# Optimization experiments

Measured on AMD Instinct MI355X. Metric: run time of the kernel, lower is better.

## Reference

```python
import jax, jax.numpy as jnp
import numpy as np

B_SZ = 4; SEQ = 2048; D_INPUT = 40; D_MODEL = 128; N_LAYERS = 4
D_STATE = 16; EXPAND = 2; D_INNER = D_MODEL * EXPAND
N_HEADS = 4; D_HEAD = D_MODEL // N_HEADS; MAX_LANDMARKS = 100
EPS_RMS = 1.1920929e-07  # torch nn.RMSNorm default eps = finfo(float32).eps
EPS_LN = 1e-5
A_FLOOR = 1e-4


def _rms(x, w):
    return x * jax.lax.rsqrt(jnp.mean(x * x, -1, keepdims=True) + EPS_RMS) * w


def _ln(x, w, b):
    m = jnp.mean(x, -1, keepdims=True)
    v = jnp.mean((x - m) ** 2, -1, keepdims=True)
    return (x - m) * jax.lax.rsqrt(v + EPS_LN) * w + b


def _mamba3_block(xin, Wi, Wx, Wdt, bdt, Alog, Bb, Cb, Bnw, Cnw, rf, Dv, Wo):
    # xin: (B,L,d_model)
    xz = xin @ Wi                       # (B,L,2*d_inner)
    xp, z = jnp.split(xz, 2, axis=-1)
    xp = jax.nn.silu(xp)
    sp = xp @ Wx                        # (B,L,2*d_state+2)
    B_raw = sp[..., :D_STATE]
    C_raw = sp[..., D_STATE:2 * D_STATE]
    dt_in = sp[..., -2:-1]
    lam_in = sp[..., -1:]
    Bm = _rms(B_raw + Bb, Bnw)
    Cm = _rms(C_raw + Cb, Cnw)
    dt = jax.nn.softplus(dt_in @ Wdt + bdt)   # (B,L,d_inner)
    lam = jax.nn.sigmoid(lam_in)              # (B,L,1)
    # data-dependent RoPE on B and C
    freqs = jax.nn.softplus(rf)                                  # (d_state//2,)
    ang = jnp.cumsum(jnp.mean(dt, -1, keepdims=True), axis=1) * freqs  # (B,L,ds/2)
    ca, sa = jnp.cos(ang), jnp.sin(ang)

    def rot(M):
        e, o = M[..., ::2], M[..., 1::2]
        return jnp.stack([e * ca - o * sa, e * sa + o * ca], -1).reshape(M.shape)

    Bm, Cm = rot(Bm), rot(Cm)
    A = jnp.minimum(-jnp.exp(Alog), -A_FLOOR)   # (d_inner,d_state)
    dte = dt[..., None]                          # (B,L,d_inner,1)
    dA = jnp.exp(A * dte)                        # (B,L,d_inner,d_state)
    Bx = Bm[:, :, None, :] * xp[..., None]       # (B,L,d_inner,d_state)
    Bx_prev = jnp.concatenate([jnp.zeros_like(Bx[:, :1]), Bx[:, :-1]], axis=1)
    lame = lam[..., None]                        # (B,L,1,1)
    u = (1.0 - lame) * dte * dA * Bx_prev + lame * dte * Bx
    u = u.at[:, 0].set(dte[:, 0] * Bx[:, 0])     # t==0 case: h = dt*B*x (no lambda)

    def step(h, inp):
        dA_t, u_t, C_t = inp
        h = dA_t * h + u_t
        return h, jnp.sum(h * C_t[:, None, :], -1)

    h0 = jnp.zeros((xin.shape[0], D_INNER, D_STATE), xin.dtype)
    _, ys = jax.lax.scan(step, h0, (jnp.swapaxes(dA, 0, 1), jnp.swapaxes(u, 0, 1), jnp.swapaxes(Cm, 0, 1)))
    y = jnp.swapaxes(ys, 0, 1)                   # (B,L,d_inner)
    y = y + xp * Dv
    y = y * jax.nn.silu(z)
    return y @ Wo


def _landmark_attn(mo, skip, hw, WQ, bQ, WK, bK, WV, bV, WO, bO):
    Bsz, L, Dm = skip.shape
    k = min(MAX_LANDMARKS, L)
    _, idx = jax.lax.top_k(hw, k)
    idx = jnp.sort(idx, axis=1)                            # (B,k)
    kv = jnp.take_along_axis(skip, idx[..., None], axis=1)  # (B,k,Dm)
    q = mo[:, -1:, :]                                       # (B,1,Dm)
    Q = (q @ WQ + bQ).reshape(Bsz, 1, N_HEADS, D_HEAD).transpose(0, 2, 1, 3)
    K = (kv @ WK + bK).reshape(Bsz, k, N_HEADS, D_HEAD).transpose(0, 2, 1, 3)
    V = (kv @ WV + bV).reshape(Bsz, k, N_HEADS, D_HEAD).transpose(0, 2, 1, 3)
    scores = jnp.einsum('bhqd,bhkd->bhqk', Q, K) * (D_HEAD ** -0.5)
    probs = jax.nn.softmax(scores, axis=-1)
    out = jnp.einsum('bhqk,bhkd->bhqd', probs, V).transpose(0, 2, 1, 3).reshape(Bsz, Dm)
    return out @ WO + bO


def setup_inputs() -> dict:
    key = jax.random.key(0)
    ks = iter(jax.random.split(key, 64))

    def nrm(shape, s=0.02):
        return jax.random.normal(next(ks), shape, jnp.float32) * s

    nl, ds, di, dm = N_LAYERS, D_STATE, D_INNER, D_MODEL
    inp = {}
    inp['x'] = jax.random.normal(next(ks), (B_SZ, SEQ, D_INPUT), jnp.float32)
    inp['hawkes_weights'] = jax.random.uniform(next(ks), (B_SZ, SEQ), jnp.float32)
    inp['emb_W'] = nrm((D_INPUT, dm)); inp['emb_b'] = jnp.zeros(dm, jnp.float32)
    inp['skip_W'] = nrm((D_INPUT, dm)); inp['skip_b'] = jnp.zeros(dm, jnp.float32)
    inp['in_proj_W'] = nrm((nl, dm, 2 * di))
    inp['x_proj_W'] = nrm((nl, di, 2 * ds + 2))
    inp['dt_proj_W'] = nrm((nl, 1, di), 1.0)
    inp['dt_proj_b'] = jnp.full((nl, di), -1.0, jnp.float32)
    inp['A_log'] = jnp.broadcast_to(jnp.log(jnp.arange(1, ds + 1, dtype=jnp.float32)), (nl, di, ds)) * jnp.ones((nl, di, ds), jnp.float32)
    inp['B_bias'] = jnp.ones((nl, ds), jnp.float32)
    inp['C_bias'] = jnp.ones((nl, ds), jnp.float32)
    inp['Bn_w'] = jnp.ones((nl, ds), jnp.float32)
    inp['Cn_w'] = jnp.ones((nl, ds), jnp.float32)
    inp['rope_freqs'] = nrm((nl, ds // 2), 0.01)
    inp['D_param'] = jnp.ones((nl, di), jnp.float32)
    inp['out_proj_W'] = nrm((nl, di, dm))
    inp['ln_w'] = jnp.ones((nl, dm), jnp.float32); inp['ln_b'] = jnp.zeros((nl, dm), jnp.float32)
    inp['fn_w'] = jnp.ones(dm, jnp.float32); inp['fn_b'] = jnp.zeros(dm, jnp.float32)
    for nm in ('Q', 'K', 'V', 'O'):
        inp['W' + nm] = nrm((dm, dm)); inp['b' + nm] = jnp.zeros(dm, jnp.float32)
    return inp


def reference(x, hawkes_weights, emb_W, emb_b, skip_W, skip_b, in_proj_W, x_proj_W,
              dt_proj_W, dt_proj_b, A_log, B_bias, C_bias, Bn_w, Cn_w, rope_freqs,
              D_param, out_proj_W, ln_w, ln_b, fn_w, fn_b, WQ, bQ, WK, bK, WV, bV, WO, bO):
    w = hawkes_weights[..., None]
    h = (x @ emb_W + emb_b) * w          # Hawkes-damped embedding for Mamba path
    skip = (x @ skip_W + skip_b) * w     # Hawkes skip for attention KV
    for i in range(N_LAYERS):
        h = h + _mamba3_block(_ln(h, ln_w[i], ln_b[i]), in_proj_W[i], x_proj_W[i],
                              dt_proj_W[i], dt_proj_b[i], A_log[i], B_bias[i], C_bias[i],
                              Bn_w[i], Cn_w[i], rope_freqs[i], D_param[i], out_proj_W[i])
    mo = _ln(h, fn_w, fn_b)
    return _landmark_attn(mo, skip, hawkes_weights, WQ, bQ, WK, bK, WV, bV, WO, bO)
```

## Files before the change

kernel.cpp:

```cpp
#include <hip/hip_runtime.h>
#include <hip/hip_fp16.h>
#include <math.h>

#define BSZ   4
#define SEQL  2048
#define DIN   40
#define DM    128
#define DI    256
#define DS    16
#define NL    4
#define NHEAD 4
#define DHEAD 32
#define KLM   100
#define NC    128
#define TC    16
#define NROWS 8
#define EROWS 16

__device__ __forceinline__ float rcp_(float x){ return __builtin_amdgcn_rcpf(x); }
__device__ __forceinline__ float sigmoidf_(float x){ return rcp_(1.0f + __expf(-x)); }
__device__ __forceinline__ float siluf_(float x){ return x*rcp_(1.0f + __expf(-x)); }
__device__ __forceinline__ float softplusf_(float x){ return fmaxf(x,0.0f) + __logf(1.0f + __expf(-fabsf(x))); }

__device__ __forceinline__ float block_sum256(float v, float* red){
  #pragma unroll
  for (int o=32;o>0;o>>=1) v += __shfl_down(v,o,64);
  __syncthreads();
  if ((threadIdx.x & 63)==0) red[threadIdx.x>>6] = v;
  __syncthreads();
  return red[0]+red[1]+red[2]+red[3];
}
__device__ __forceinline__ void load8(const float* p, float* r){
  const float4* q = (const float4*)p;
  float4 a=q[0], b=q[1];
  r[0]=a.x;r[1]=a.y;r[2]=a.z;r[3]=a.w; r[4]=b.x;r[5]=b.y;r[6]=b.z;r[7]=b.w;
}
__device__ __forceinline__ void store8(float* p, const float* r){
  float4* q = (float4*)p;
  q[0]=make_float4(r[0],r[1],r[2],r[3]);  q[1]=make_float4(r[4],r[5],r[6],r[7]);
}
__device__ __forceinline__ void load16(const float* p, float* r){
  load8(p, r); load8(p+8, r+8);
}
__device__ __forceinline__ void store16(float* p, const float* r){
  store8(p, r); store8(p+8, r+8);
}

__global__ __launch_bounds__(256) void embed_kernel(
    const float* __restrict__ x, const float* __restrict__ hw,
    const float* __restrict__ eW, const float* __restrict__ eb,
    const float* __restrict__ sW, const float* __restrict__ sb,
    float* __restrict__ hb, float* __restrict__ sk)
{
  __shared__ float xr[EROWS][DIN];
  const int t = threadIdx.x;
  const size_t R0 = (size_t)blockIdx.x * EROWS;
  for (int e=t; e<EROWS*DIN; e+=256) ((float*)xr)[e] = x[R0*DIN + e];
  __syncthreads();
  const int c = t & (DM-1), g = t >> 7;
  float ae[8], as[8];
  #pragma unroll
  for (int j=0;j<8;j++){ ae[j]=0.0f; as[j]=0.0f; }
  for (int k=0;k<DIN;k++){
    const float we  = eW[(size_t)k*DM + c];
    const float ws_ = sW[(size_t)k*DM + c];
    #pragma unroll
    for (int j=0;j<8;j++){
      const float xv = xr[g*8+j][k];
      ae[j] = fmaf(xv, we, ae[j]);
      as[j] = fmaf(xv, ws_, as[j]);
    }
  }
  const float ebv = eb[c], sbv = sb[c];
  #pragma unroll
  for (int j=0;j<8;j++){
    const size_t R = R0 + g*8 + j;
    const float w = hw[R];
    hb[R*DM + c] = (ae[j]+ebv)*w;
    sk[R*DM + c] = (as[j]+sbv)*w;
  }
}

__global__ __launch_bounds__(256) void pre_kernel(
    const float* __restrict__ hb,
    const float* __restrict__ Wi, const float* __restrict__ Wx,
    const float* __restrict__ Wdt, const float* __restrict__ bdt,
    const float* __restrict__ Bb, const float* __restrict__ Cb,
    const float* __restrict__ Bnw, const float* __restrict__ Cnw,
    const float* __restrict__ lnw, const float* __restrict__ lnb,
    __half* __restrict__ xph, __half* __restrict__ zsh,
    float* __restrict__ dtin, float* __restrict__ Shalf,
    float* __restrict__ Bmb, float* __restrict__ Cmb,
    float* __restrict__ lamb, float* __restrict__ mdtb)
{
  __shared__ float xin[NROWS][DM+4];
  __shared__ float xps[NROWS][DI+4];
  __shared__ float spl[NROWS][40];
  __shared__ float pr[NROWS][4];

  const int t = threadIdx.x;
  const size_t R0 = (size_t)blockIdx.x * NROWS;

  {
    const int r = t >> 5, j = t & 31;
    const float4 v = ((const float4*)(hb + (R0 + r)*DM))[j];
    float s = v.x+v.y+v.z+v.w;
    #pragma unroll
    for (int o=16;o>0;o>>=1) s += __shfl_xor(s,o,32);
    const float m = s*(1.0f/DM);
    const float dx=v.x-m, dy=v.y-m, dz=v.z-m, dw=v.w-m;
    float ss = dx*dx+dy*dy+dz*dz+dw*dw;
    #pragma unroll
    for (int o=16;o>0;o>>=1) ss += __shfl_xor(ss,o,32);
    const float inv = 1.0f/sqrtf(ss*(1.0f/DM) + 1e-5f);
    const int c = j*4;
    xin[r][c+0] = dx*inv*lnw[c+0] + lnb[c+0];
    xin[r][c+1] = dy*inv*lnw[c+1] + lnb[c+1];
    xin[r][c+2] = dz*inv*lnw[c+2] + lnb[c+2];
    xin[r][c+3] = dw*inv*lnw[c+3] + lnb[c+3];
  }
  __syncthreads();

  {
    float2 a[NROWS];
    #pragma unroll
    for (int r=0;r<NROWS;r++){ a[r].x=0.0f; a[r].y=0.0f; }
    for (int k=0;k<DM;k+=4){
      const float2 w0 = *(const float2*)&Wi[(size_t)(k+0)*(2*DI) + 2*t];
      const float2 w1 = *(const float2*)&Wi[(size_t)(k+1)*(2*DI) + 2*t];
      const float2 w2 = *(const float2*)&Wi[(size_t)(k+2)*(2*DI) + 2*t];
      const float2 w3 = *(const float2*)&Wi[(size_t)(k+3)*(2*DI) + 2*t];
      #pragma unroll
      for (int r=0;r<NROWS;r++){
        const float4 xv = *(const float4*)&xin[r][k];
        a[r].x = fmaf(xv.x,w0.x,a[r].x); a[r].y = fmaf(xv.x,w0.y,a[r].y);
        a[r].x = fmaf(xv.y,w1.x,a[r].x); a[r].y = fmaf(xv.y,w1.y,a[r].y);
        a[r].x = fmaf(xv.z,w2.x,a[r].x); a[r].y = fmaf(xv.z,w2.y,a[r].y);
        a[r].x = fmaf(xv.w,w3.x,a[r].x); a[r].y = fmaf(xv.w,w3.y,a[r].y);
      }
    }
    if (t < 128){
      #pragma unroll
      for (int r=0;r<NROWS;r++){
        const float sx = siluf_(a[r].x), sy = siluf_(a[r].y);
        xps[r][2*t] = sx; xps[r][2*t+1] = sy;
        *(__half2*)&xph[(R0+r)*DI + 2*t] =
            __halves2half2(__float2half_rn(sx), __float2half_rn(sy));
      }
    } else {
      const int zc = 2*t - 2*DI + DI;
      #pragma unroll
      for (int r=0;r<NROWS;r++){
        const float sx = siluf_(a[r].x), sy = siluf_(a[r].y);
        *(__half2*)&zsh[(R0+r)*DI + zc] =
            __halves2half2(__float2half_rn(sx), __float2half_rn(sy));
      }
    }
  }
  __syncthreads();

  if (t < 136){
    const int r = t & 7, op = t >> 3;
    float ax=0.0f, ay=0.0f;
    for (int k=0;k<DI;k+=4){
      const float4 xv = *(const float4*)&xps[r][k];
      const float2 w0 = *(const float2*)&Wx[(size_t)(k+0)*34 + 2*op];
      const float2 w1 = *(const float2*)&Wx[(size_t)(k+1)*34 + 2*op];
      const float2 w2 = *(const float2*)&Wx[(size_t)(k+2)*34 + 2*op];
      const float2 w3 = *(const float2*)&Wx[(size_t)(k+3)*34 + 2*op];
      ax = fmaf(xv.x,w0.x,ax); ay = fmaf(xv.x,w0.y,ay);
      ax = fmaf(xv.y,w1.x,ax); ay = fmaf(xv.y,w1.y,ay);
      ax = fmaf(xv.z,w2.x,ax); ay = fmaf(xv.z,w2.y,ay);
      ax = fmaf(xv.w,w3.x,ax); ay = fmaf(xv.w,w3.y,ay);
    }
    spl[r][2*op] = ax; spl[r][2*op+1] = ay;
  }
  __syncthreads();

  {
    const int half = t >> 7;
    const int r2 = (t >> 4) & 7, s2 = t & 15;
    const float* bias = half ? Cb : Bb;
    const float* wn   = half ? Cnw : Bnw;
    const float v = spl[r2][half*DS + s2] + bias[s2];
    float ss = v*v;
    #pragma unroll
    for (int o=8;o>0;o>>=1) ss += __shfl_xor(ss,o,16);
    const float inv = 1.0f/sqrtf(ss*(1.0f/DS) + 1.1920929e-07f);
    (half ? Cmb : Bmb)[(R0+r2)*DS + s2] = v*inv*wn[s2];
  }

  {
    const int lane = t & 63, w = t >> 6;
    const float wdt = Wdt[t], bdtv = bdt[t];
    float Sd = 0.0f;
    #pragma unroll
    for (int r=0;r<NROWS;r++){
      const float dval = softplusf_(fmaf(spl[r][32], wdt, bdtv));
      Sd += dval;
      float s = dval;
      #pragma unroll
      for (int o=32;o>0;o>>=1) s += __shfl_xor(s,o,64);
      if (lane==0) pr[r][w] = s;
    }
    Shalf[(size_t)blockIdx.x * DI + t] = Sd;
    if (t < NROWS){
      lamb[R0+t] = sigmoidf_(spl[t][33]);
      dtin[R0+t] = spl[t][32];
    }
  }
  __syncthreads();
  if (t < NROWS)
    mdtb[R0+t] = (pr[t][0]+pr[t][1]+pr[t][2]+pr[t][3])*(1.0f/DI);
}

__global__ __launch_bounds__(256) void cumsum_kernel(
    const float* __restrict__ mdt, double* __restrict__ csum_g)
{
  __shared__ double wsum[4];
  const int b = blockIdx.x, t = threadIdx.x;
  const int lane = t & 63, w = t >> 6;
  const float* p = mdt + (size_t)b*SEQL + (size_t)t*8;
  double v[8]; double s = 0.0;
  #pragma unroll
  for (int q=0;q<8;q++){ v[q] = (double)p[q]; s += v[q]; }
  double sc = s;
  #pragma unroll
  for (int o=1;o<64;o<<=1){
    const double nb = __shfl_up(sc, o, 64);
    if (lane >= o) sc += nb;
  }
  if (lane==63) wsum[w] = sc;
  __syncthreads();
  double woff = 0.0;
  for (int j=0;j<w;j++) woff += wsum[j];
  double run = woff + sc - s;
  double* dst = csum_g + (size_t)b*SEQL + (size_t)t*8;
  #pragma unroll
  for (int q=0;q<8;q++){ run += v[q]; dst[q] = run; }
}

__global__ __launch_bounds__(256) void csfill_kernel(
    const double* __restrict__ csum_g, const float* __restrict__ rf,
    float2* __restrict__ cst)
{
  __shared__ double fqs[8];
  const int t = threadIdx.x;
  if (t < 8){
    const double xfr = (double)rf[t];
    fqs[t] = fmax(xfr, 0.0) + log1p(exp(-fabs(xfr)));
  }
  __syncthreads();
  const int row = blockIdx.x*256 + t;
  const double ab = csum_g[row];
  const double TWO_PI = 6.283185307179586;
  const double INV2PI = 0.15915494309189535;
  float2 o8[8];
  #pragma unroll
  for (int f=0; f<8; f++){
    const double ang = ab * fqs[f];
    const double red = ang - floor(ang*INV2PI)*TWO_PI;
    float sa, ca;
    __sincosf((float)red, &sa, &ca);
    o8[f] = make_float2(ca, sa);
  }
  float4* dst = (float4*)&cst[(size_t)row*8];
  dst[0] = make_float4(o8[0].x,o8[0].y,o8[1].x,o8[1].y);
  dst[1] = make_float4(o8[2].x,o8[2].y,o8[3].x,o8[3].y);
  dst[2] = make_float4(o8[4].x,o8[4].y,o8[5].x,o8[5].y);
  dst[3] = make_float4(o8[6].x,o8[6].y,o8[7].x,o8[7].y);
}

__global__ __launch_bounds__(512) void scan1_kernel(
    const __half* __restrict__ xph, const float* __restrict__ dtin,
    const float* __restrict__ Wdt, const float* __restrict__ bdt,
    const float* __restrict__ Bmb, const float* __restrict__ lamb,
    const float2* __restrict__ cst,
    const float* __restrict__ Alog, float* __restrict__ hend)
{
  __shared__ float Bst[TC+1][DS];
  __shared__ float lst[TC];
  __shared__ float dsl[TC];
  __shared__ __half xpl[TC+1][DI+8];
  const int t = threadIdx.x;
  const int d  = t >> 1;
  const int s0 = (t & 1) * 8;
  const int c = blockIdx.x & (NC-1);
  const int b = blockIdx.x >> 7;
  const size_t bL = (size_t)b*SEQL;
  const int t0 = c*TC;
  const int id = blockIdx.x*256 + d;

  for (int e=t; e<(TC+1)*DS; e+=512){
    const int j = e >> 4, s = e & 15;
    const int trow = t0 - 1 + j;
    Bst[j][s] = (trow >= 0) ? Bmb[(bL + trow)*DS + s] : 0.0f;
  }
  for (int e=t; e<(TC+1)*DI; e+=512){
    const int j = e >> 8, dd = e & (DI-1);
    const int trow = t0 - 1 + j;
    xpl[j][dd] = (trow >= 0) ? xph[(bL + trow)*DI + dd] : __float2half_rn(0.0f);
  }
  if (t < TC){
    lst[t] = lamb[bL + t0 + t];
    dsl[t] = dtin[bL + t0 + t];
  }
  __syncthreads();
  if (t < 136){
    const int j = t >> 3, f = t & 7;
    const int trow = t0 - 1 + j;
    if (trow >= 0){
      const float2 cs = cst[((size_t)(bL + trow))*8 + f];
      const float e0 = Bst[j][2*f], o0 = Bst[j][2*f+1];
      Bst[j][2*f]   = e0*cs.x - o0*cs.y;
      Bst[j][2*f+1] = e0*cs.y + o0*cs.x;
    }
  }
  __syncthreads();

  float A[8];
  #pragma unroll
  for (int s=0;s<8;s++) A[s] = fminf(-__expf(Alog[d*DS + s0 + s]), -1e-4f);
  const float wdt = Wdt[d], bdtv = bdt[d];
  float h[8], Bprev[8];
  #pragma unroll
  for (int s=0;s<8;s++) h[s]=0.0f;
  float xpm1;
  int tstart;
  if (t0 > 0){
    #pragma unroll
    for (int s=0;s<8;s++) Bprev[s] = Bst[0][s0+s];
    xpm1 = __half2float(xpl[0][d]);
    tstart = t0;
  } else {
    const float dtv = softplusf_(fmaf(dsl[0], wdt, bdtv));
    const float xpv = __half2float(xpl[1][d]);
    #pragma unroll
    for (int s=0;s<8;s++){
      h[s] = dtv*(Bst[1][s0+s]*xpv);
      Bprev[s] = Bst[1][s0+s];
    }
    xpm1 = xpv;
    tstart = 1;
  }
  for (int tt=tstart; tt<t0+TC; ++tt){
    const int j = tt - t0;
    const float dtv = softplusf_(fmaf(dsl[j], wdt, bdtv));
    const float xpv = __half2float(xpl[j+1][d]);
    const float lamv = lst[j];
    const float dl = dtv*lamv;
    const float dml = dtv - dl;
    #pragma unroll
    for (int s=0;s<8;s++){
      const float a = __expf(A[s]*dtv);
      const float Bc = Bst[j+1][s0+s];
      const float u = fmaf(dml*a, Bprev[s]*xpm1, dl*(Bc*xpv));
      h[s] = fmaf(a, h[s], u);
      Bprev[s] = Bc;
    }
    xpm1 = xpv;
  }
  store8(hend + (size_t)id*DS + s0, h);
}

__global__ __launch_bounds__(128) void scan2_kernel(
    float* __restrict__ hend, const float* __restrict__ Shalf,
    const float* __restrict__ Alog)
{
  __shared__ float hS[NC][DS+1];
  __shared__ float pS[NC][DS+1];
  const int c = threadIdx.x;
  const int d = blockIdx.x & (DI-1);
  const int b = blockIdx.x >> 8;
  const float S = Shalf[(size_t)(b*(SEQL/NROWS) + 2*c)*DI + d]
                + Shalf[(size_t)(b*(SEQL/NROWS) + 2*c + 1)*DI + d];
  float P[DS], h[DS];
  #pragma unroll
  for (int s=0;s<DS;s++){
    const float A = fminf(-__expf(Alog[d*DS+s]), -1e-4f);
    P[s] = __expf(A*S);
  }
  load16(hend + (((size_t)(b*NC + c))*DI + d)*DS, h);
  #pragma unroll
  for (int s=0;s<DS;s++){ hS[c][s]=h[s]; pS[c][s]=P[s]; }
  __syncthreads();
  for (int off=1; off<NC; off<<=1){
    float hn[DS], pn[DS];
    const int src = c - off;
    if (src >= 0){
      #pragma unroll
      for (int s=0;s<DS;s++){ hn[s]=hS[src][s]; pn[s]=pS[src][s]; }
    }
    __syncthreads();
    if (src >= 0){
      #pragma unroll
      for (int s=0;s<DS;s++){
        h[s] = fmaf(P[s], hn[s], h[s]);
        P[s] *= pn[s];
        hS[c][s] = h[s]; pS[c][s] = P[s];
      }
    }
    __syncthreads();
  }
  float o[DS];
  if (c == 0){
    #pragma unroll
    for (int s=0;s<DS;s++) o[s] = 0.0f;
  } else {
    #pragma unroll
    for (int s=0;s<DS;s++) o[s] = hS[c-1][s];
  }
  store16(hend + (((size_t)(b*NC + c))*DI + d)*DS, o);
}

__global__ __launch_bounds__(512) void scan3post_kernel(
    const __half* __restrict__ xph, const float* __restrict__ dtin,
    const float* __restrict__ Wdt, const float* __restrict__ bdt,
    const float* __restrict__ Bmb, const float* __restrict__ Cmb,
    const float* __restrict__ lamb, const __half* __restrict__ zsh,
    const float2* __restrict__ cst,
    const float* __restrict__ Alog, const float* __restrict__ Dv,
    const float* __restrict__ Hin, const float* __restrict__ Wo,
    float* __restrict__ hb)
{
  __shared__ float Bst[TC+1][DS];
  __shared__ float Cst[TC][DS];
  __shared__ float lst[TC];
  __shared__ float dsl[TC];
  __shared__ __half xpl[TC+1][DI+8];
  __shared__ __half zsl[TC][DI+8];
  __shared__ float ys[TC][DI+4];
  const int t = threadIdx.x;
  const int d  = t >> 1;
  const int sh = t & 1;
  const int s0 = sh * 8;
  const int c = blockIdx.x & (NC-1);
  const int b = blockIdx.x >> 7;
  const size_t bL = (size_t)b*SEQL;
  const int t0 = c*TC;
  const int id = blockIdx.x*256 + d;

  for (int e=t; e<(TC+1)*DS; e+=512){
    const int j = e >> 4, s = e & 15;
    const int trow = t0 - 1 + j;
    Bst[j][s] = (trow >= 0) ? Bmb[(bL + trow)*DS + s] : 0.0f;
    if (j < TC) Cst[j][s] = Cmb[(bL + t0 + j)*DS + s];
  }
  for (int e=t; e<(TC+1)*DI; e+=512){
    const int j = e >> 8, dd = e & (DI-1);
    const int trow = t0 - 1 + j;
    xpl[j][dd] = (trow >= 0) ? xph[(bL + trow)*DI + dd] : __float2half_rn(0.0f);
    if (j < TC) zsl[j][dd] = zsh[(bL + t0 + j)*DI + dd];
  }
  if (t < TC){
    lst[t] = lamb[bL + t0 + t];
    dsl[t] = dtin[bL + t0 + t];
  }
  __syncthreads();
  if (t < 264){
    if (t < 136){
      const int j = t >> 3, f = t & 7;
      const int trow = t0 - 1 + j;
      if (trow >= 0){
        const float2 cs = cst[((size_t)(bL + trow))*8 + f];
        const float e0 = Bst[j][2*f], o0 = Bst[j][2*f+1];
        Bst[j][2*f]   = e0*cs.x - o0*cs.y;
        Bst[j][2*f+1] = e0*cs.y + o0*cs.x;
      }
    } else {
      const int e2 = t - 136;
      const int j = e2 >> 3, f = e2 & 7;
      const float2 cs = cst[((size_t)(bL + t0 + j))*8 + f];
      const float e0 = Cst[j][2*f], o0 = Cst[j][2*f+1];
      Cst[j][2*f]   = e0*cs.x - o0*cs.y;
      Cst[j][2*f+1] = e0*cs.y + o0*cs.x;
    }
  }
  __syncthreads();

  float A[8];
  #pragma unroll
  for (int s=0;s<8;s++) A[s] = fminf(-__expf(Alog[d*DS + s0 + s]), -1e-4f);
  const float wdt = Wdt[d], bdtv = bdt[d];
  const float dvp = Dv[d];
  float h[8], Bprev[8];
  load8(Hin + (size_t)id*DS + s0, h);
  float xpm1;
  int tstart;
  if (t0 > 0){
    #pragma unroll
    for (int s=0;s<8;s++) Bprev[s] = Bst[0][s0+s];
    xpm1 = __half2float(xpl[0][d]);
    tstart = t0;
  } else {
    const float dtv = softplusf_(fmaf(dsl[0], wdt, bdtv));
    const float xpv = __half2float(xpl[1][d]);
    float y = 0.0f;
    #pragma unroll
    for (int s=0;s<8;s++){
      h[s] = dtv*(Bst[1][s0+s]*xpv);
      y = fmaf(h[s], Cst[0][s0+s], y);
      Bprev[s] = Bst[1][s0+s];
    }
    const float ytot = y + __shfl_xor(y, 1, 64);
    if (sh == 0) ys[0][d] = (ytot + xpv*dvp)*__half2float(zsl[0][d]);
    xpm1 = xpv;
    tstart = 1;
  }
  for (int tt=tstart; tt<t0+TC; ++tt){
    const int j = tt - t0;
    const float dtv = softplusf_(fmaf(dsl[j], wdt, bdtv));
    const float xpv = __half2float(xpl[j+1][d]);
    const float lamv = lst[j];
    const float dl = dtv*lamv;
    const float dml = dtv - dl;
    float y = 0.0f;
    #pragma unroll
    for (int s=0;s<8;s++){
      const float a = __expf(A[s]*dtv);
      const float Bc = Bst[j+1][s0+s];
      const float u = fmaf(dml*a, Bprev[s]*xpm1, dl*(Bc*xpv));
      h[s] = fmaf(a, h[s], u);
      y = fmaf(h[s], Cst[j][s0+s], y);
      Bprev[s] = Bc;
    }
    const float ytot = y + __shfl_xor(y, 1, 64);
    if (sh == 0) ys[j][d] = (ytot + xpv*dvp)*__half2float(zsl[j][d]);
    xpm1 = xpv;
  }
  __syncthreads();

  {
    const int r  = t >> 5;
    const int cg = t & 31;
    const int c0 = cg*4;
    float acc[4] = {0.0f,0.0f,0.0f,0.0f};
    for (int k=0;k<DI;k+=4){
      const float4 yv = *(const float4*)&ys[r][k];
      const float yy[4] = {yv.x, yv.y, yv.z, yv.w};
      #pragma unroll
      for (int j=0;j<4;j++){
        const float4 wa = *(const float4*)&Wo[(size_t)(k+j)*DM + c0];
        acc[0]=fmaf(yy[j],wa.x,acc[0]); acc[1]=fmaf(yy[j],wa.y,acc[1]);
        acc[2]=fmaf(yy[j],wa.z,acc[2]); acc[3]=fmaf(yy[j],wa.w,acc[3]);
      }
    }
    const size_t row = bL + t0 + r;
    float4 h0 = *(const float4*)&hb[row*DM + c0];
    h0.x+=acc[0]; h0.y+=acc[1]; h0.z+=acc[2]; h0.w+=acc[3];
    *(float4*)&hb[row*DM + c0] = h0;
  }
}

__global__ __launch_bounds__(256) void topk_kernel(
    const float* __restrict__ hb, const float* __restrict__ hw,
    const float* __restrict__ fnw, const float* __restrict__ fnb,
    int* __restrict__ idxl_g, float* __restrict__ mog)
{
  __shared__ int redcnt[2][4];
  __shared__ int eqc[8][4], gtc[8][4];
  __shared__ float red_f[4];

  const int b = blockIdx.x;
  const int t = threadIdx.x;
  const int lane = t & 63, w = t >> 6;

  const float* hwp = hw + (size_t)b*SEQL;
  unsigned vb[8];
  #pragma unroll
  for (int q=0;q<8;q++) vb[q] = __float_as_uint(hwp[q*256 + t]);

  unsigned kth = 0u;
  for (int bit=31; bit>=0; --bit){
    const unsigned cand = kth | (1u << bit);
    int c0 = 0;
    #pragma unroll
    for (int q=0;q<8;q++) c0 += __popcll(__ballot(vb[q] >= cand));
    const int par = bit & 1;
    if (lane == 0) redcnt[par][w] = c0;
    __syncthreads();
    const int tot = redcnt[par][0]+redcnt[par][1]+redcnt[par][2]+redcnt[par][3];
    if (tot >= KLM) kth = cand;
  }

  unsigned long long beq[8], bgt[8];
  #pragma unroll
  for (int q=0;q<8;q++){
    beq[q] = __ballot(vb[q] == kth);
    bgt[q] = __ballot(vb[q] >  kth);
  }
  if (lane == 0){
    #pragma unroll
    for (int q=0;q<8;q++){ eqc[q][w] = __popcll(beq[q]); gtc[q][w] = __popcll(bgt[q]); }
  }
  __syncthreads();
  {
    int gtTot = 0;
    #pragma unroll
    for (int q=0;q<8;q++) gtTot += gtc[q][0]+gtc[q][1]+gtc[q][2]+gtc[q][3];
    const int need_eq = KLM - gtTot;
    const unsigned long long lmask = (lane==0) ? 0ull : ((~0ull) >> (64-lane));
    int eqPfx = 0, gtPfx = 0;
    #pragma unroll
    for (int q=0;q<8;q++){
      int eqWP = 0, gtWP = 0;
      for (int w2=0; w2<w; ++w2){ eqWP += eqc[q][w2]; gtWP += gtc[q][w2]; }
      const int eqBefore = eqPfx + eqWP + __popcll(beq[q] & lmask);
      const int gtBefore = gtPfx + gtWP + __popcll(bgt[q] & lmask);
      if (vb[q] > kth){
        const int pos = gtBefore + min(eqBefore, need_eq);
        if (pos < KLM) idxl_g[b*KLM + pos] = q*256 + t;
      } else if (vb[q] == kth && eqBefore < need_eq){
        const int pos = gtBefore + eqBefore;
        if (pos < KLM) idxl_g[b*KLM + pos] = q*256 + t;
      }
      eqPfx += eqc[q][0]+eqc[q][1]+eqc[q][2]+eqc[q][3];
      gtPfx += gtc[q][0]+gtc[q][1]+gtc[q][2]+gtc[q][3];
    }
  }

  {
    const float* hr = hb + ((size_t)b*SEQL + (SEQL-1))*DM;
    const float hv = (t < DM) ? hr[t] : 0.0f;
    const float ssum = block_sum256(hv, red_f);
    const float mean = ssum*(1.0f/DM);
    const float dv = (t < DM) ? (hv - mean) : 0.0f;
    const float vsum = block_sum256(dv*dv, red_f);
    const float inv = 1.0f/sqrtf(vsum*(1.0f/DM) + 1e-5f);
    if (t < DM) mog[b*DM + t] = dv*inv*fnw[t] + fnb[t];
  }
}

__global__ __launch_bounds__(256) void attnmid_kernel(
    const float* __restrict__ sk, const int* __restrict__ idxl_g,
    const float* __restrict__ mog,
    const float* __restrict__ WQ, const float* __restrict__ bQ,
    const float* __restrict__ WK, const float* __restrict__ bK,
    const float* __restrict__ WV, const float* __restrict__ bV,
    float* __restrict__ attnog)
{
  __shared__ float kv[KLM][DM+4];
  __shared__ float Qs[DHEAD];
  __shared__ float qk[DM];
  __shared__ float sc[KLM];
  __shared__ float pbar[DM];
  __shared__ float bterm_s;
  const int t = threadIdx.x;
  const int b = blockIdx.x >> 2, hh = blockIdx.x & 3;
  const int c0 = hh*DHEAD;

  for (int e=t; e<KLM*DM; e+=256){
    const int j = e >> 7, cc = e & (DM-1);
    kv[j][cc] = sk[((size_t)b*SEQL + idxl_g[b*KLM + j])*DM + cc];
  }
  if (t < DHEAD){
    float a = bQ[c0+t];
    #pragma unroll 4
    for (int k=0;k<DM;k++) a = fmaf(mog[b*DM+k], WQ[(size_t)k*DM + c0+t], a);
    Qs[t] = a;
  }
  __syncthreads();
  if (t < DM){
    float a = 0.0f;
    #pragma unroll
    for (int cc=0; cc<DHEAD; cc++) a = fmaf(WK[(size_t)t*DM + c0 + cc], Qs[cc], a);
    qk[t] = a;
  } else if (t == DM){
    float a = 0.0f;
    for (int cc=0; cc<DHEAD; cc++) a += bK[c0+cc]*Qs[cc];
    bterm_s = a;
  }
  __syncthreads();
  if (t < KLM){
    float a = bterm_s;
    for (int m=0;m<DM;m+=4){
      const float4 kvv = *(const float4*)&kv[t][m];
      const float4 qv  = *(const float4*)&qk[m];
      a = fmaf(kvv.x,qv.x,a); a = fmaf(kvv.y,qv.y,a);
      a = fmaf(kvv.z,qv.z,a); a = fmaf(kvv.w,qv.w,a);
    }
    sc[t] = a*0.17677669529663687f;
  }
  __syncthreads();
  if (t < 64){
    const int lane = t;
    const float v0 = (lane < KLM) ? sc[lane] : -3.0e38f;
    const float v1 = (lane+64 < KLM) ? sc[lane+64] : -3.0e38f;
    float mx = fmaxf(v0, v1);
    #pragma unroll
    for (int o2=32;o2>0;o2>>=1) mx = fmaxf(mx, __shfl_xor(mx,o2,64));
    const float e0 = (lane < KLM) ? __expf(v0-mx) : 0.0f;
    const float e1 = (lane+64 < KLM) ? __expf(v1-mx) : 0.0f;
    float sm = e0+e1;
    #pragma unroll
    for (int o2=32;o2>0;o2>>=1) sm += __shfl_xor(sm,o2,64);
    const float inv2 = rcp_(sm);
    if (lane < KLM) sc[lane] = e0*inv2;
    if (lane+64 < KLM) sc[lane+64] = e1*inv2;
  }
  __syncthreads();
  if (t < DM){
    float a = 0.0f;
    #pragma unroll 4
    for (int j=0;j<KLM;j++) a = fmaf(sc[j], kv[j][t], a);
    pbar[t] = a;
  }
  __syncthreads();
  if (t < DHEAD){
    const int cc = c0 + t;
    float a = bV[cc];
    #pragma unroll 4
    for (int m=0;m<DM;m++) a = fmaf(pbar[m], WV[(size_t)m*DM + cc], a);
    attnog[b*DM + cc] = a;
  }
}

__global__ __launch_bounds__(128) void attnout_kernel(
    const float* __restrict__ attnog, const float* __restrict__ WO,
    const float* __restrict__ bO, float* __restrict__ outp)
{
  __shared__ float ao[DM];
  const int b = blockIdx.x, t = threadIdx.x;
  ao[t] = attnog[b*DM + t];
  __syncthreads();
  float a = bO[t];
  #pragma unroll 4
  for (int c2=0;c2<DM;c2++) a = fmaf(ao[c2], WO[(size_t)c2*DM + t], a);
  outp[(size_t)b*DM + t] = a;
}

extern "C" void kernel_launch(void* const* d_in, const int* in_sizes, int n_in,
                              void* d_out, int out_size, void* d_ws, size_t ws_size,
                              hipStream_t stream)
{
  (void)in_sizes; (void)n_in; (void)out_size; (void)ws_size;
  const float* x    = (const float*)d_in[0];
  const float* hw   = (const float*)d_in[1];
  const float* embW = (const float*)d_in[2];
  const float* embB = (const float*)d_in[3];
  const float* skW  = (const float*)d_in[4];
  const float* skB  = (const float*)d_in[5];
  const float* inW  = (const float*)d_in[6];
  const float* xpW  = (const float*)d_in[7];
  const float* dtW  = (const float*)d_in[8];
  const float* dtB  = (const float*)d_in[9];
  const float* Alog = (const float*)d_in[10];
  const float* Bb   = (const float*)d_in[11];
  const float* Cb   = (const float*)d_in[12];
  const float* Bnw  = (const float*)d_in[13];
  const float* Cnw  = (const float*)d_in[14];
  const float* rf   = (const float*)d_in[15];
  const float* Dpar = (const float*)d_in[16];
  const float* outW = (const float*)d_in[17];
  const float* lnW  = (const float*)d_in[18];
  const float* lnB  = (const float*)d_in[19];
  const float* fnW  = (const float*)d_in[20];
  const float* fnB  = (const float*)d_in[21];
  const float* WQ = (const float*)d_in[22]; const float* bQ = (const float*)d_in[23];
  const float* WK = (const float*)d_in[24]; const float* bK = (const float*)d_in[25];
  const float* WV = (const float*)d_in[26]; const float* bV = (const float*)d_in[27];
  const float* WO = (const float*)d_in[28]; const float* bO = (const float*)d_in[29];

  float* ws = (float*)d_ws;
  size_t off = 0;
  float* hb    = ws + off; off += (size_t)BSZ*SEQL*DM;
  float* sk    = ws + off; off += (size_t)BSZ*SEQL*DM;
  __half* xph  = (__half*)(ws + off); off += (size_t)BSZ*SEQL*DI/2;
  __half* zsh  = (__half*)(ws + off); off += (size_t)BSZ*SEQL*DI/2;
  float* Bmb   = ws + off; off += (size_t)BSZ*SEQL*DS;
  float* Cmb   = ws + off; off += (size_t)BSZ*SEQL*DS;
  float* lamb  = ws + off; off += (size_t)BSZ*SEQL;
  float* mdtb  = ws + off; off += (size_t)BSZ*SEQL;
  float* dtin  = ws + off; off += (size_t)BSZ*SEQL;
  float* Shalf = ws + off; off += (size_t)BSZ*(SEQL/NROWS)*DI;
  float* hend  = ws + off; off += (size_t)BSZ*NC*DI*DS;
  float2* cst  = (float2*)(ws + off); off += (size_t)BSZ*SEQL*16;
  double* csum_g = (double*)(ws + off); off += (size_t)BSZ*SEQL*2;
  int* idxl_g  = (int*)(ws + off); off += (size_t)BSZ*KLM;
  float* mog   = ws + off; off += (size_t)BSZ*DM;
  float* attnog= ws + off; off += (size_t)BSZ*DM;

  embed_kernel<<<BSZ*SEQL/EROWS, 256, 0, stream>>>(x, hw, embW, embB, skW, skB, hb, sk);

  for (int i=0;i<NL;i++){
    pre_kernel<<<BSZ*SEQL/NROWS, 256, 0, stream>>>(hb,
        inW + (size_t)i*DM*2*DI, xpW + (size_t)i*DI*34,
        dtW + (size_t)i*DI, dtB + (size_t)i*DI,
        Bb + i*DS, Cb + i*DS, Bnw + i*DS, Cnw + i*DS,
        lnW + i*DM, lnB + i*DM,
        xph, zsh, dtin, Shalf, Bmb, Cmb, lamb, mdtb);
    cumsum_kernel<<<BSZ, 256, 0, stream>>>(mdtb, csum_g);
    csfill_kernel<<<BSZ*SEQL/256, 256, 0, stream>>>(csum_g, rf + i*8, cst);
    scan1_kernel<<<BSZ*NC, 512, 0, stream>>>(xph, dtin,
        dtW + (size_t)i*DI, dtB + (size_t)i*DI,
        Bmb, lamb, cst, Alog + (size_t)i*DI*DS, hend);
    scan2_kernel<<<BSZ*DI, 128, 0, stream>>>(hend, Shalf, Alog + (size_t)i*DI*DS);
    scan3post_kernel<<<BSZ*NC, 512, 0, stream>>>(xph, dtin,
        dtW + (size_t)i*DI, dtB + (size_t)i*DI,
        Bmb, Cmb, lamb, zsh, cst,
        Alog + (size_t)i*DI*DS, Dpar + (size_t)i*DI, hend,
        outW + (size_t)i*DI*DM, hb);
  }

  topk_kernel<<<BSZ, 256, 0, stream>>>(hb, hw, fnW, fnB, idxl_g, mog);
  attnmid_kernel<<<BSZ*NHEAD, 256, 0, stream>>>(sk, idxl_g, mog,
      WQ, bQ, WK, bK, WV, bV, attnog);
  attnout_kernel<<<BSZ, 128, 0, stream>>>(attnog, WO, bO, (float*)d_out);
}
```

Measured before the change: 576.3 us.

## Retile scan3 out-projection, split topk from final LayerNorm, simplify scan loops

The scan3post out-projection moves from one row per 32 threads to 4x4 register tiles. The K dimension is split across two thread halves and combined through a shared-memory reduction that reuses the ys buffer, which gives more reuse of each Wo load. Top-k selection now runs first, since it depends only on the Hawkes weights, and the final LayerNorm moves into attnmid, which drops one kernel boundary and the mog buffer. The scan loops are also rewritten over local indices. The extra syncs and the shared-memory aliasing add some overhead and correctness risk.

```diff
diff --git a/kernel.cpp b/kernel.cpp
--- a/kernel.cpp
+++ b/kernel.cpp
@@ -22,14 +22,6 @@
 __device__ __forceinline__ float siluf_(float x){ return x*rcp_(1.0f + __expf(-x)); }
 __device__ __forceinline__ float softplusf_(float x){ return fmaxf(x,0.0f) + __logf(1.0f + __expf(-fabsf(x))); }
 
-__device__ __forceinline__ float block_sum256(float v, float* red){
-  #pragma unroll
-  for (int o=32;o>0;o>>=1) v += __shfl_down(v,o,64);
-  __syncthreads();
-  if ((threadIdx.x & 63)==0) red[threadIdx.x>>6] = v;
-  __syncthreads();
-  return red[0]+red[1]+red[2]+red[3];
-}
 __device__ __forceinline__ void load8(const float* p, float* r){
   const float4* q = (const float4*)p;
   float4 a=q[0], b=q[1];
@@ -44,6 +36,71 @@
 }
 __device__ __forceinline__ void store16(float* p, const float* r){
   store8(p, r); store8(p+8, r+8);
+}
+
+__global__ __launch_bounds__(256) void topk_kernel(
+    const float* __restrict__ hw, int* __restrict__ idxl_g)
+{
+  __shared__ int redcnt[2][4];
+  __shared__ int eqc[8][4], gtc[8][4];
+
+  const int b = blockIdx.x;
+  const int t = threadIdx.x;
+  const int lane = t & 63, w = t >> 6;
+
+  const float* hwp = hw + (size_t)b*SEQL;
+  unsigned vb[8];
+  #pragma unroll
+  for (int q=0;q<8;q++) vb[q] = __float_as_uint(hwp[q*256 + t]);
+
+  unsigned kth = 0u;
+  for (int bit=31; bit>=0; --bit){
+    const unsigned cand = kth | (1u << bit);
+    int c0 = 0;
+    #pragma unroll
+    for (int q=0;q<8;q++) c0 += __popcll(__ballot(vb[q] >= cand));
+    const int par = bit & 1;
+    if (lane == 0) redcnt[par][w] = c0;
+    __syncthreads();
+    const int tot = redcnt[par][0]+redcnt[par][1]+redcnt[par][2]+redcnt[par][3];
+    if (tot >= KLM) kth = cand;
+  }
+
+  unsigned long long beq[8], bgt[8];
+  #pragma unroll
+  for (int q=0;q<8;q++){
+    beq[q] = __ballot(vb[q] == kth);
+    bgt[q] = __ballot(vb[q] >  kth);
+  }
+  if (lane == 0){
+    #pragma unroll
+    for (int q=0;q<8;q++){ eqc[q][w] = __popcll(beq[q]); gtc[q][w] = __popcll(bgt[q]); }
+  }
+  __syncthreads();
+  {
+    int gtTot = 0;
+    #pragma unroll
+    for (int q=0;q<8;q++) gtTot += gtc[q][0]+gtc[q][1]+gtc[q][2]+gtc[q][3];
+    const int need_eq = KLM - gtTot;
+    const unsigned long long lmask = (lane==0) ? 0ull : ((~0ull) >> (64-lane));
+    int eqPfx = 0, gtPfx = 0;
+    #pragma unroll
+    for (int q=0;q<8;q++){
+      int eqWP = 0, gtWP = 0;
+      for (int w2=0; w2<w; ++w2){ eqWP += eqc[q][w2]; gtWP += gtc[q][w2]; }
+      const int eqBefore = eqPfx + eqWP + __popcll(beq[q] & lmask);
+      const int gtBefore = gtPfx + gtWP + __popcll(bgt[q] & lmask);
+      if (vb[q] > kth){
+        const int pos = gtBefore + min(eqBefore, need_eq);
+        if (pos < KLM) idxl_g[b*KLM + pos] = q*256 + t;
+      } else if (vb[q] == kth && eqBefore < need_eq){
+        const int pos = gtBefore + eqBefore;
+        if (pos < KLM) idxl_g[b*KLM + pos] = q*256 + t;
+      }
+      eqPfx += eqc[q][0]+eqc[q][1]+eqc[q][2]+eqc[q][3];
+      gtPfx += gtc[q][0]+gtc[q][1]+gtc[q][2]+gtc[q][3];
+    }
+  }
 }
 
 __global__ __launch_bounds__(256) void embed_kernel(
@@ -331,7 +388,7 @@
     #pragma unroll
     for (int s=0;s<8;s++) Bprev[s] = Bst[0][s0+s];
     xpm1 = __half2float(xpl[0][d]);
-    tstart = t0;
+    tstart = 0;
   } else {
     const float dtv = softplusf_(fmaf(dsl[0], wdt, bdtv));
     const float xpv = __half2float(xpl[1][d]);
@@ -343,8 +400,7 @@
     xpm1 = xpv;
     tstart = 1;
   }
-  for (int tt=tstart; tt<t0+TC; ++tt){
-    const int j = tt - t0;
+  for (int j=tstart; j<TC; ++j){
     const float dtv = softplusf_(fmaf(dsl[j], wdt, bdtv));
     const float xpv = __half2float(xpl[j+1][d]);
     const float lamv = lst[j];
@@ -491,7 +547,7 @@
     #pragma unroll
     for (int s=0;s<8;s++) Bprev[s] = Bst[0][s0+s];
     xpm1 = __half2float(xpl[0][d]);
-    tstart = t0;
+    tstart = 0;
   } else {
     const float dtv = softplusf_(fmaf(dsl[0], wdt, bdtv));
     const float xpv = __half2float(xpl[1][d]);
@@ -507,8 +563,7 @@
     xpm1 = xpv;
     tstart = 1;
   }
-  for (int tt=tstart; tt<t0+TC; ++tt){
-    const int j = tt - t0;
+  for (int j=tstart; j<TC; ++j){
     const float dtv = softplusf_(fmaf(dsl[j], wdt, bdtv));
     const float xpv = __half2float(xpl[j+1][d]);
     const float lamv = lst[j];
@@ -531,115 +586,76 @@
   __syncthreads();
 
   {
-    const int r  = t >> 5;
-    const int cg = t & 31;
-    const int c0 = cg*4;
-    float acc[4] = {0.0f,0.0f,0.0f,0.0f};
-    for (int k=0;k<DI;k+=4){
-      const float4 yv = *(const float4*)&ys[r][k];
-      const float yy[4] = {yv.x, yv.y, yv.z, yv.w};
+    const int cg2  = t & 31;
+    const int ks2  = (t >> 5) & 1;
+    const int rg   = (t >> 6) & 3;
+    const int ksHi = t >> 8;
+    const int seg = ksHi*2 + ks2;
+    const int k0 = seg*64;
+    const int c0c = cg2*4;
+    float acc[4][4];
+    #pragma unroll
+    for (int rr=0;rr<4;rr++){ acc[rr][0]=0.f; acc[rr][1]=0.f; acc[rr][2]=0.f; acc[rr][3]=0.f; }
+    for (int k=k0; k<k0+64; k+=4){
+      float4 yv[4];
+      #pragma unroll
+      for (int rr=0;rr<4;rr++) yv[rr] = *(const float4*)&ys[rg*4+rr][k];
       #pragma unroll
       for (int j=0;j<4;j++){
-        const float4 wa = *(const float4*)&Wo[(size_t)(k+j)*DM + c0];
-        acc[0]=fmaf(yy[j],wa.x,acc[0]); acc[1]=fmaf(yy[j],wa.y,acc[1]);
-        acc[2]=fmaf(yy[j],wa.z,acc[2]); acc[3]=fmaf(yy[j],wa.w,acc[3]);
+        const float4 wv = *(const float4*)&Wo[(size_t)(k+j)*DM + c0c];
+        const float y0 = (j==0)?yv[0].x:(j==1)?yv[0].y:(j==2)?yv[0].z:yv[0].w;
+        const float y1 = (j==0)?yv[1].x:(j==1)?yv[1].y:(j==2)?yv[1].z:yv[1].w;
+        const float y2 = (j==0)?yv[2].x:(j==1)?yv[2].y:(j==2)?yv[2].z:yv[2].w;
+        const float y3 = (j==0)?yv[3].x:(j==1)?yv[3].y:(j==2)?yv[3].z:yv[3].w;
+        acc[0][0]=fmaf(y0,wv.x,acc[0][0]); acc[0][1]=fmaf(y0,wv.y,acc[0][1]);
+        acc[0][2]=fmaf(y0,wv.z,acc[0][2]); acc[0][3]=fmaf(y0,wv.w,acc[0][3]);
+        acc[1][0]=fmaf(y1,wv.x,acc[1][0]); acc[1][1]=fmaf(y1,wv.y,acc[1][1]);
+        acc[1][2]=fmaf(y1,wv.z,acc[1][2]); acc[1][3]=fmaf(y1,wv.w,acc[1][3]);
+        acc[2][0]=fmaf(y2,wv.x,acc[2][0]); acc[2][1]=fmaf(y2,wv.y,acc[2][1]);
+        acc[2][2]=fmaf(y2,wv.z,acc[2][2]); acc[2][3]=fmaf(y2,wv.w,acc[2][3]);
+        acc[3][0]=fmaf(y3,wv.x,acc[3][0]); acc[3][1]=fmaf(y3,wv.y,acc[3][1]);
+        acc[3][2]=fmaf(y3,wv.z,acc[3][2]); acc[3][3]=fmaf(y3,wv.w,acc[3][3]);
       }
     }
-    const size_t row = bL + t0 + r;
-    float4 h0 = *(const float4*)&hb[row*DM + c0];
-    h0.x+=acc[0]; h0.y+=acc[1]; h0.z+=acc[2]; h0.w+=acc[3];
-    *(float4*)&hb[row*DM + c0] = h0;
-  }
-}
-
-__global__ __launch_bounds__(256) void topk_kernel(
-    const float* __restrict__ hb, const float* __restrict__ hw,
+    #pragma unroll
+    for (int rr=0;rr<4;rr++){
+      #pragma unroll
+      for (int cc=0;cc<4;cc++) acc[rr][cc] += __shfl_down(acc[rr][cc], 32, 64);
+    }
+    float (*red)[132] = (float(*)[132])ys;
+    __syncthreads();
+    const int lane = t & 63;
+    if (ksHi == 1 && lane < 32){
+      #pragma unroll
+      for (int rr=0;rr<4;rr++)
+        *(float4*)&red[rg*4+rr][c0c] = make_float4(acc[rr][0],acc[rr][1],acc[rr][2],acc[rr][3]);
+    }
+    __syncthreads();
+    if (ksHi == 0 && lane < 32){
+      #pragma unroll
+      for (int rr=0;rr<4;rr++){
+        const float4 rv = *(const float4*)&red[rg*4+rr][c0c];
+        const size_t row = bL + t0 + rg*4 + rr;
+        float4 hv = *(const float4*)&hb[row*DM + c0c];
+        hv.x += acc[rr][0] + rv.x; hv.y += acc[rr][1] + rv.y;
+        hv.z += acc[rr][2] + rv.z; hv.w += acc[rr][3] + rv.w;
+        *(float4*)&hb[row*DM + c0c] = hv;
+      }
+    }
+  }
+}
+
+__global__ __launch_bounds__(256) void attnmid_kernel(
+    const float* __restrict__ hb, const float* __restrict__ sk,
+    const int* __restrict__ idxl_g,
     const float* __restrict__ fnw, const float* __restrict__ fnb,
-    int* __restrict__ idxl_g, float* __restrict__ mog)
-{
-  __shared__ int redcnt[2][4];
-  __shared__ int eqc[8][4], gtc[8][4];
-  __shared__ float red_f[4];
-
-  const int b = blockIdx.x;
-  const int t = threadIdx.x;
-  const int lane = t & 63, w = t >> 6;
-
-  const float* hwp = hw + (size_t)b*SEQL;
-  unsigned vb[8];
-  #pragma unroll
-  for (int q=0;q<8;q++) vb[q] = __float_as_uint(hwp[q*256 + t]);
-
-  unsigned kth = 0u;
-  for (int bit=31; bit>=0; --bit){
-    const unsigned cand = kth | (1u << bit);
-    int c0 = 0;
-    #pragma unroll
-    for (int q=0;q<8;q++) c0 += __popcll(__ballot(vb[q] >= cand));
-    const int par = bit & 1;
-    if (lane == 0) redcnt[par][w] = c0;
-    __syncthreads();
-    const int tot = redcnt[par][0]+redcnt[par][1]+redcnt[par][2]+redcnt[par][3];
-    if (tot >= KLM) kth = cand;
-  }
-
-  unsigned long long beq[8], bgt[8];
-  #pragma unroll
-  for (int q=0;q<8;q++){
-    beq[q] = __ballot(vb[q] == kth);
-    bgt[q] = __ballot(vb[q] >  kth);
-  }
-  if (lane == 0){
-    #pragma unroll
-    for (int q=0;q<8;q++){ eqc[q][w] = __popcll(beq[q]); gtc[q][w] = __popcll(bgt[q]); }
-  }
-  __syncthreads();
-  {
-    int gtTot = 0;
-    #pragma unroll
-    for (int q=0;q<8;q++) gtTot += gtc[q][0]+gtc[q][1]+gtc[q][2]+gtc[q][3];
-    const int need_eq = KLM - gtTot;
-    const unsigned long long lmask = (lane==0) ? 0ull : ((~0ull) >> (64-lane));
-    int eqPfx = 0, gtPfx = 0;
-    #pragma unroll
-    for (int q=0;q<8;q++){
-      int eqWP = 0, gtWP = 0;
-      for (int w2=0; w2<w; ++w2){ eqWP += eqc[q][w2]; gtWP += gtc[q][w2]; }
-      const int eqBefore = eqPfx + eqWP + __popcll(beq[q] & lmask);
-      const int gtBefore = gtPfx + gtWP + __popcll(bgt[q] & lmask);
-      if (vb[q] > kth){
-        const int pos = gtBefore + min(eqBefore, need_eq);
-        if (pos < KLM) idxl_g[b*KLM + pos] = q*256 + t;
-      } else if (vb[q] == kth && eqBefore < need_eq){
-        const int pos = gtBefore + eqBefore;
-        if (pos < KLM) idxl_g[b*KLM + pos] = q*256 + t;
-      }
-      eqPfx += eqc[q][0]+eqc[q][1]+eqc[q][2]+eqc[q][3];
-      gtPfx += gtc[q][0]+gtc[q][1]+gtc[q][2]+gtc[q][3];
-    }
-  }
-
-  {
-    const float* hr = hb + ((size_t)b*SEQL + (SEQL-1))*DM;
-    const float hv = (t < DM) ? hr[t] : 0.0f;
-    const float ssum = block_sum256(hv, red_f);
-    const float mean = ssum*(1.0f/DM);
-    const float dv = (t < DM) ? (hv - mean) : 0.0f;
-    const float vsum = block_sum256(dv*dv, red_f);
-    const float inv = 1.0f/sqrtf(vsum*(1.0f/DM) + 1e-5f);
-    if (t < DM) mog[b*DM + t] = dv*inv*fnw[t] + fnb[t];
-  }
-}
-
-__global__ __launch_bounds__(256) void attnmid_kernel(
-    const float* __restrict__ sk, const int* __restrict__ idxl_g,
-    const float* __restrict__ mog,
     const float* __restrict__ WQ, const float* __restrict__ bQ,
     const float* __restrict__ WK, const float* __restrict__ bK,
     const float* __restrict__ WV, const float* __restrict__ bV,
     float* __restrict__ attnog)
 {
   __shared__ float kv[KLM][DM+4];
+  __shared__ float mo[DM];
   __shared__ float Qs[DHEAD];
   __shared__ float qk[DM];
   __shared__ float sc[KLM];
@@ -649,14 +665,30 @@
   const int b = blockIdx.x >> 2, hh = blockIdx.x & 3;
   const int c0 = hh*DHEAD;
 
+  if (t < 64){
+    const float* hr = hb + ((size_t)b*SEQL + (SEQL-1))*DM;
+    const float v0 = hr[t], v1 = hr[t+64];
+    float s = v0+v1;
+    #pragma unroll
+    for (int o=32;o>0;o>>=1) s += __shfl_xor(s,o,64);
+    const float m = s*(1.0f/DM);
+    const float d0=v0-m, d1=v1-m;
+    float ss = d0*d0 + d1*d1;
+    #pragma unroll
+    for (int o=32;o>0;o>>=1) ss += __shfl_xor(ss,o,64);
+    const float inv = 1.0f/sqrtf(ss*(1.0f/DM) + 1e-5f);
+    mo[t]    = d0*inv*fnw[t]    + fnb[t];
+    mo[t+64] = d1*inv*fnw[t+64] + fnb[t+64];
+  }
   for (int e=t; e<KLM*DM; e+=256){
     const int j = e >> 7, cc = e & (DM-1);
     kv[j][cc] = sk[((size_t)b*SEQL + idxl_g[b*KLM + j])*DM + cc];
   }
+  __syncthreads();
   if (t < DHEAD){
     float a = bQ[c0+t];
     #pragma unroll 4
-    for (int k=0;k<DM;k++) a = fmaf(mog[b*DM+k], WQ[(size_t)k*DM + c0+t], a);
+    for (int k=0;k<DM;k++) a = fmaf(mo[k], WQ[(size_t)k*DM + c0+t], a);
     Qs[t] = a;
   }
   __syncthreads();
@@ -777,9 +809,9 @@
   float2* cst  = (float2*)(ws + off); off += (size_t)BSZ*SEQL*16;
   double* csum_g = (double*)(ws + off); off += (size_t)BSZ*SEQL*2;
   int* idxl_g  = (int*)(ws + off); off += (size_t)BSZ*KLM;
-  float* mog   = ws + off; off += (size_t)BSZ*DM;
   float* attnog= ws + off; off += (size_t)BSZ*DM;
 
+  topk_kernel<<<BSZ, 256, 0, stream>>>(hw, idxl_g);
   embed_kernel<<<BSZ*SEQL/EROWS, 256, 0, stream>>>(x, hw, embW, embB, skW, skB, hb, sk);
 
   for (int i=0;i<NL;i++){
@@ -802,8 +834,7 @@
         outW + (size_t)i*DI*DM, hb);
   }
 
-  topk_kernel<<<BSZ, 256, 0, stream>>>(hb, hw, fnW, fnB, idxl_g, mog);
-  attnmid_kernel<<<BSZ*NHEAD, 256, 0, stream>>>(sk, idxl_g, mog,
+  attnmid_kernel<<<BSZ*NHEAD, 256, 0, stream>>>(hb, sk, idxl_g, fnW, fnB,
       WQ, bQ, WK, bK, WV, bV, attnog);
   attnout_kernel<<<BSZ, 128, 0, stream>>>(attnog, WO, bO, (float*)d_out);
 }
```

Measured after the change: 506.7 us. 1.14x faster.
